# Kernel tuning notes

Measured on AMD Instinct MI355X. Metric: run time of the kernel, lower is better.

The kernel has to match this reference:

```python
import jax, jax.numpy as jnp
import numpy as np

NEG_SLOPE = 0.2


def _segment_softmax(scores, seg, num_segments):
    # scores: [nnz, H]; segment-wise (scatter) softmax, matching torch_geometric.utils.softmax
    m = jax.ops.segment_max(scores, seg, num_segments=num_segments)
    m = jnp.where(jnp.isfinite(m), m, 0.0)  # empty segments
    e = jnp.exp(scores - m[seg])
    s = jax.ops.segment_sum(e, seg, num_segments=num_segments)
    return e / (s[seg] + 1e-16)


def _class_partition(key, nnz, heads):
    # random permutation split into 4 class groups + inverse-permutation gather index
    perm = jax.random.permutation(key, nnz).astype(jnp.int32)
    q = nnz // 4
    parts = (perm[:q], perm[q:2 * q], perm[2 * q:3 * q], perm[3 * q:])
    inv = jnp.zeros((nnz,), jnp.int32).at[perm].set(jnp.arange(nnz, dtype=jnp.int32))
    gather_idx = jnp.broadcast_to(inv[:, None], (nnz, heads))
    return parts, gather_idx


def setup_inputs() -> dict:
    key = jax.random.key(0)
    N, M, NNZ = 100000, 50000, 800000
    IN_C, H, C = 128, 8, 16
    ks = jax.random.split(key, 9)
    X = jax.random.normal(ks[0], (N, IN_C), jnp.float32)
    vertex = jax.random.randint(ks[1], (NNZ,), 0, N, dtype=jnp.int32)
    edges = jax.random.randint(ks[2], (NNZ,), 0, M, dtype=jnp.int32)
    W_w = jax.random.normal(ks[3], (IN_C, H * C), jnp.float32) / np.float32(np.sqrt(IN_C))
    W_b = jnp.zeros((H * C,), jnp.float32)
    stdv = np.float32(np.sqrt(6.0 / (H + C)))
    att_e = jax.random.uniform(ks[4], (1, H, C), jnp.float32, -stdv, stdv)
    att_v = jax.random.uniform(ks[5], (1, H, C), jnp.float32, -stdv, stdv)
    (E0, E1, E2, E3), E_idx = _class_partition(ks[6], NNZ, H)
    (V0, V1, V2, V3), V_idx = _class_partition(ks[7], NNZ, H)
    return dict(X=X, vertex=vertex, edges=edges, W_w=W_w, W_b=W_b,
                att_e=att_e, att_v=att_v,
                E_class_index_0=E0, E_class_index_1=E1, E_class_index_2=E2, E_class_index_3=E3,
                E_class_index=E_idx,
                V_class_index_0=V0, V_class_index_1=V1, V_class_index_2=V2, V_class_index_3=V3,
                V_class_index=V_idx, edge_num=M)


def _class_scores(Xg, att, idx0, idx1, idx2, idx3):
    # (index_select by class, dot with att, sum over channel) then concat -> [nnz, H]
    parts = [jnp.sum(Xg[i] * att, axis=-1) for i in (idx0, idx1, idx2, idx3)]
    return jnp.concatenate(parts, axis=0)


def reference(X, vertex, edges, W_w, W_b, att_e, att_v,
              E_class_index_0, E_class_index_1, E_class_index_2, E_class_index_3, E_class_index,
              V_class_index_0, V_class_index_1, V_class_index_2, V_class_index_3, V_class_index,
              edge_num):
    N = X.shape[0]
    H, C = att_e.shape[1], att_e.shape[2]
    X0 = X @ W_w + W_b                       # [N, H*C]
    Xn = X0.reshape(N, H, C)
    Xve = Xn[vertex]                          # [nnz, H, C] gather node feats per incidence

    # vertex -> edge attention (edge-type-classed scores, segment softmax over hyperedges)
    Xe_cat = _class_scores(Xve, att_e, E_class_index_0, E_class_index_1, E_class_index_2, E_class_index_3)
    beta = jnp.take_along_axis(Xe_cat, E_class_index, axis=0)   # restore incidence order
    beta = jax.nn.leaky_relu(beta, NEG_SLOPE)
    beta = _segment_softmax(beta, edges, edge_num)              # [nnz, H]
    Xe = jax.ops.segment_sum(Xve * beta[..., None], edges, num_segments=edge_num)  # [M, H, C]
    Xe = jax.nn.relu(Xe)[edges]                                  # gather back: [nnz, H, C]

    # edge -> vertex attention (node-type-classed scores, segment softmax over vertices)
    Xa_cat = _class_scores(Xe, att_v, V_class_index_0, V_class_index_1, V_class_index_2, V_class_index_3)
    alpha = jnp.take_along_axis(Xa_cat, V_class_index, axis=0)
    alpha = jax.nn.leaky_relu(alpha, NEG_SLOPE)
    alpha = _segment_softmax(alpha, vertex, N)                   # [nnz, H]
    Xv = jax.ops.segment_sum(Xe * alpha[..., None], vertex, num_segments=N)  # [N, H, C]
    return Xv.reshape(N, H * C)
```

## Files before the change

### kernel.cpp

```cpp
#include <hip/hip_runtime.h>
#include <cstdint>
#include <cmath>

#define NEG_SLOPE 0.2f

static __device__ __forceinline__ float leaky(float x){ return x >= 0.f ? x : NEG_SLOPE*x; }

__global__ __launch_bounds__(256) void hist_rank_k(const int* __restrict__ edges, const int* __restrict__ vertex,
                                                   int* __restrict__ ce, int* __restrict__ cv,
                                                   int* __restrict__ re, int* __restrict__ rv, int nnz){
  int i = blockIdx.x*256 + threadIdx.x;
  if (i < nnz){
    re[i] = atomicAdd(&ce[edges[i]], 1);
    rv[i] = atomicAdd(&cv[vertex[i]], 1);
  }
}

__global__ __launch_bounds__(256) void scan_reduce_k(const int* __restrict__ ce, const int* __restrict__ cv,
                                                     int M, int N, int* __restrict__ partials){
  const int* src = blockIdx.y ? cv : ce;
  const int L = blockIdx.y ? N : M;
  const int base = blockIdx.x*2048;
  int s = 0;
  for (int j = threadIdx.x; j < 2048; j += 256){
    int idx = base + j;
    if (idx < L) s += src[idx];
  }
  for (int o = 32; o > 0; o >>= 1) s += __shfl_down(s, o);
  __shared__ int wsum[4];
  if ((threadIdx.x & 63) == 0) wsum[threadIdx.x >> 6] = s;
  __syncthreads();
  if (threadIdx.x == 0) partials[blockIdx.y*64 + blockIdx.x] = wsum[0]+wsum[1]+wsum[2]+wsum[3];
}

__global__ __launch_bounds__(128) void scan_partials_k(int* __restrict__ partials){
  const int w = threadIdx.x >> 6, l = threadIdx.x & 63;
  int v = partials[w*64 + l];
  int inc = v;
  for (int o = 1; o < 64; o <<= 1){ int u = __shfl_up(inc, o); if (l >= o) inc += u; }
  partials[w*64 + l] = inc - v;
}

__global__ __launch_bounds__(256) void scan_write_k(const int* __restrict__ ce, const int* __restrict__ cv,
                                                    int M, int N, const int* __restrict__ partials,
                                                    int* __restrict__ e_off, int* __restrict__ v_off){
  const int* src; int L; int* off;
  if (blockIdx.y == 0){ src = ce; L = M; off = e_off; }
  else                { src = cv; L = N; off = v_off; }
  const int base = blockIdx.x*2048 + threadIdx.x*8;
  int v[8];
  int tot = 0;
  #pragma unroll
  for (int j = 0; j < 8; ++j){ int idx = base+j; v[j] = (idx < L) ? src[idx] : 0; tot += v[j]; }
  const int lane = threadIdx.x & 63, wid = threadIdx.x >> 6;
  int inc = tot;
  for (int o = 1; o < 64; o <<= 1){ int u = __shfl_up(inc, o); if (lane >= o) inc += u; }
  __shared__ int wsum[4];
  if (lane == 63) wsum[wid] = inc;
  __syncthreads();
  int wbase = 0;
  for (int k = 0; k < wid; ++k) wbase += wsum[k];
  int run = partials[blockIdx.y*64 + blockIdx.x] + wbase + inc - tot;
  #pragma unroll
  for (int j = 0; j < 8; ++j){
    int idx = base + j;
    if (idx < L){
      off[idx] = run;
      run += v[j];
      if (idx == L-1) off[L] = run;
    }
  }
}

__global__ __launch_bounds__(256) void place_k(const int* __restrict__ edges, const int* __restrict__ vertex,
                                               const int* __restrict__ e_off, const int* __restrict__ v_off,
                                               const int* __restrict__ re, const int* __restrict__ rv,
                                               int* __restrict__ e_ent, int* __restrict__ v_ent, int nnz){
  int i = blockIdx.x*256 + threadIdx.x;
  if (i < nnz){
    atomicExch(&e_ent[e_off[edges[i]] + re[i]], i);
    atomicExch(&v_ent[v_off[vertex[i]] + rv[i]], i);
  }
}

__global__ __launch_bounds__(512) void gemm_k(const float* __restrict__ X, const float* __restrict__ W,
                                              const float* __restrict__ bias, const float* __restrict__ att_e,
                                              float* __restrict__ Y, float* __restrict__ sc_n, int N){
  __shared__ float Bs[64*128];
  __shared__ float As[64*65];
  __shared__ float att_s[128];
  const int t = threadIdx.x;
  if (t < 128) att_s[t] = att_e[t];
  const int row0 = blockIdx.x * 64;
  const int tr = t >> 4, tc = t & 15;
  const int r = tr*2, c = tc*8;
  float acc[2][8];
  {
    float4 b0 = ((const float4*)bias)[tc*2];
    float4 b1 = ((const float4*)bias)[tc*2+1];
    acc[0][0]=b0.x; acc[0][1]=b0.y; acc[0][2]=b0.z; acc[0][3]=b0.w;
    acc[0][4]=b1.x; acc[0][5]=b1.y; acc[0][6]=b1.z; acc[0][7]=b1.w;
    #pragma unroll
    for (int j = 0; j < 8; ++j) acc[1][j] = acc[0][j];
  }
  for (int kh = 0; kh < 2; ++kh){
    {
      const float4* W4 = (const float4*)(W + kh*64*128);
      float4* B4 = (float4*)Bs;
      #pragma unroll
      for (int j = 0; j < 4; ++j) B4[j*512 + t] = W4[j*512 + t];
      #pragma unroll
      for (int j = 0; j < 2; ++j){
        int idx = j*512 + t;
        int rr = idx >> 4, c4 = idx & 15;
        int gr = row0 + rr;
        float4 v = make_float4(0.f,0.f,0.f,0.f);
        if (gr < N) v = ((const float4*)X)[(size_t)gr*32 + kh*16 + c4];
        float* dst = &As[rr*65 + c4*4];
        dst[0]=v.x; dst[1]=v.y; dst[2]=v.z; dst[3]=v.w;
      }
    }
    __syncthreads();
    #pragma unroll 4
    for (int k = 0; k < 64; ++k){
      float a0 = As[r*65 + k], a1 = As[(r+1)*65 + k];
      const float4 w0 = *(const float4*)&Bs[k*128 + c];
      const float4 w1 = *(const float4*)&Bs[k*128 + c + 4];
      float wv[8] = {w0.x,w0.y,w0.z,w0.w,w1.x,w1.y,w1.z,w1.w};
      #pragma unroll
      for (int j = 0; j < 8; ++j){ acc[0][j] += a0*wv[j]; acc[1][j] += a1*wv[j]; }
    }
    __syncthreads();
  }
  float p0 = 0.f, p1 = 0.f;
  #pragma unroll
  for (int j = 0; j < 8; ++j){ p0 += acc[0][j]*att_s[c+j]; p1 += acc[1][j]*att_s[c+j]; }
  p0 += __shfl_xor(p0, 1);
  p1 += __shfl_xor(p1, 1);
  #pragma unroll
  for (int i = 0; i < 2; ++i){
    int gr = row0 + r + i;
    if (gr < N){
      float4 o0 = make_float4(acc[i][0],acc[i][1],acc[i][2],acc[i][3]);
      float4 o1 = make_float4(acc[i][4],acc[i][5],acc[i][6],acc[i][7]);
      float4* Y4 = (float4*)Y;
      Y4[(size_t)gr*32 + tc*2]     = o0;
      Y4[(size_t)gr*32 + tc*2 + 1] = o1;
    }
  }
  if ((tc & 1) == 0){
    int h = tc >> 1;
    int g0 = row0 + r, g1 = row0 + r + 1;
    if (g0 < N) sc_n[(size_t)g0*8 + h] = leaky(p0);
    if (g1 < N) sc_n[(size_t)g1*8 + h] = leaky(p1);
  }
}

template<bool RELU_SCORE>
__global__ __launch_bounds__(256) void agg_k(const float* __restrict__ src, const int* __restrict__ map,
                                             const float* __restrict__ sctab, const int* __restrict__ seg_off,
                                             const int* __restrict__ seg_ent, const float* __restrict__ att2,
                                             float* __restrict__ out, float* __restrict__ sc_out, int nseg){
  __shared__ float s_lds[4][128][8];
  __shared__ int   r_lds[4][128];
  __shared__ float m_lds[4][8];
  __shared__ float d_lds[4][8];
  __shared__ float att_s[128];
  const int wid = threadIdx.x >> 6, lane = threadIdx.x & 63;
  if (RELU_SCORE && threadIdx.x < 128) att_s[threadIdx.x] = att2[threadIdx.x];
  const int seg = blockIdx.x*4 + wid;
  const bool active = seg < nseg;
  int start = 0, cnt = 0;
  if (active){ start = seg_off[seg]; cnt = seg_off[seg+1] - start; }
  const bool fits = (cnt <= 128);

  if (active && fits){
    for (int j = lane; j < cnt; j += 64){
      int id = seg_ent[start + j];
      int row = map[id];
      r_lds[wid][j] = row;
      const float4* sp = (const float4*)(sctab + (size_t)row*8);
      float4 x0 = sp[0], x1 = sp[1];
      float* dst = &s_lds[wid][j][0];
      ((float4*)dst)[0] = x0;
      ((float4*)dst)[1] = x1;
    }
  }
  __syncthreads();
  if (active && fits){
    const int h = lane & 7, jj = lane >> 3;
    float m = -INFINITY;
    for (int j = jj; j < cnt; j += 8) m = fmaxf(m, s_lds[wid][j][h]);
    #pragma unroll
    for (int o = 8; o < 64; o <<= 1) m = fmaxf(m, __shfl_xor(m, o));
    float s = 0.f;
    for (int j = jj; j < cnt; j += 8) s += __expf(s_lds[wid][j][h] - m);
    #pragma unroll
    for (int o = 8; o < 64; o <<= 1) s += __shfl_xor(s, o);
    if (lane < 8){ m_lds[wid][lane] = m; d_lds[wid][lane] = 1.f / (s + 1e-16f); }
  }
  __syncthreads();
  if (active && fits){
    for (int idx = lane; idx < cnt*8; idx += 64){
      int j = idx >> 3, h = idx & 7;
      s_lds[wid][j][h] = __expf(s_lds[wid][j][h] - m_lds[wid][h]) * d_lds[wid][h];
    }
  }
  __syncthreads();
  if (active){
    float acc0 = 0.f, acc1 = 0.f;
    const int ha = lane >> 4, hb = ha + 4;
    if (fits){
      for (int j = 0; j < cnt; ++j){
        float wa = s_lds[wid][j][ha];
        float wb = s_lds[wid][j][hb];
        const float* xr = src + (size_t)r_lds[wid][j]*128;
        acc0 += wa * xr[lane];
        acc1 += wb * xr[lane + 64];
      }
    } else {
      float ma = -INFINITY, mb = -INFINITY;
      for (int j = 0; j < cnt; ++j){
        int id = seg_ent[start + j];
        int row = map[id];
        ma = fmaxf(ma, sctab[(size_t)row*8 + ha]);
        mb = fmaxf(mb, sctab[(size_t)row*8 + hb]);
      }
      float sa = 0.f, sb = 0.f;
      for (int j = 0; j < cnt; ++j){
        int id = seg_ent[start + j];
        int row = map[id];
        sa += __expf(sctab[(size_t)row*8 + ha] - ma);
        sb += __expf(sctab[(size_t)row*8 + hb] - mb);
      }
      float ra = 1.f/(sa + 1e-16f), rb = 1.f/(sb + 1e-16f);
      for (int j = 0; j < cnt; ++j){
        int id = seg_ent[start + j];
        int row = map[id];
        float wa = __expf(sctab[(size_t)row*8 + ha] - ma) * ra;
        float wb = __expf(sctab[(size_t)row*8 + hb] - mb) * rb;
        const float* xr = src + (size_t)row*128;
        acc0 += wa * xr[lane];
        acc1 += wb * xr[lane + 64];
      }
    }
    float o0 = RELU_SCORE ? fmaxf(acc0, 0.f) : acc0;
    float o1 = RELU_SCORE ? fmaxf(acc1, 0.f) : acc1;
    out[(size_t)seg*128 + lane]      = o0;
    out[(size_t)seg*128 + 64 + lane] = o1;
    if (RELU_SCORE){
      float p0 = o0 * att_s[lane];
      float p1 = o1 * att_s[lane + 64];
      #pragma unroll
      for (int o = 1; o < 16; o <<= 1){ p0 += __shfl_xor(p0, o); p1 += __shfl_xor(p1, o); }
      if ((lane & 15) == 0){
        sc_out[(size_t)seg*8 + (lane >> 4)]     = leaky(p0);
        sc_out[(size_t)seg*8 + 4 + (lane >> 4)] = leaky(p1);
      }
    }
  }
}

extern "C" void kernel_launch(void* const* d_in, const int* in_sizes, int n_in,
                              void* d_out, int out_size, void* d_ws, size_t ws_size,
                              hipStream_t stream){
  const float* X      = (const float*)d_in[0];
  const int*   vertex = (const int*)d_in[1];
  const int*   edges  = (const int*)d_in[2];
  const float* W_w    = (const float*)d_in[3];
  const float* W_b    = (const float*)d_in[4];
  const float* att_e  = (const float*)d_in[5];
  const float* att_v  = (const float*)d_in[6];
  const int N   = in_sizes[0] / 128;
  const int NNZ = in_sizes[1];
  const int M   = 50000;

  char* p = (char*)d_ws;
  auto take = [&](size_t bytes)->void*{
    void* q = (void*)p;
    p += (bytes + 255) & ~(size_t)255;
    return q;
  };
  float* X0       = (float*)take((size_t)N*128*sizeof(float));
  float* Xe       = (float*)take((size_t)M*128*sizeof(float));
  float* sc_n     = (float*)take((size_t)N*8*sizeof(float));
  float* sc_e     = (float*)take((size_t)M*8*sizeof(float));
  int*   e_off    = (int*)take((size_t)(M+1)*sizeof(int));
  int*   v_off    = (int*)take((size_t)(N+1)*sizeof(int));
  int*   e_cnt    = (int*)take((size_t)M*sizeof(int));
  int*   v_cnt    = (int*)take((size_t)N*sizeof(int));
  int*   re       = (int*)take((size_t)NNZ*sizeof(int));
  int*   rv       = (int*)take((size_t)NNZ*sizeof(int));
  int*   e_ent    = (int*)take((size_t)NNZ*sizeof(int));
  int*   v_ent    = (int*)take((size_t)NNZ*sizeof(int));
  int*   partials = (int*)take(128*sizeof(int));

  hipMemsetAsync(e_cnt, 0, (size_t)M*sizeof(int), stream);
  hipMemsetAsync(v_cnt, 0, (size_t)N*sizeof(int), stream);

  gemm_k<<<dim3((N+63)/64), 512, 0, stream>>>(X, W_w, W_b, att_e, X0, sc_n, N);

  hist_rank_k<<<dim3((NNZ+255)/256), 256, 0, stream>>>(edges, vertex, e_cnt, v_cnt, re, rv, NNZ);
  const int LMAX = (N > M) ? N : M;
  const int nb = (LMAX + 2047)/2048;
  scan_reduce_k<<<dim3(nb,2), 256, 0, stream>>>(e_cnt, v_cnt, M, N, partials);
  scan_partials_k<<<dim3(1), 128, 0, stream>>>(partials);
  scan_write_k<<<dim3(nb,2), 256, 0, stream>>>(e_cnt, v_cnt, M, N, partials, e_off, v_off);
  place_k<<<dim3((NNZ+255)/256), 256, 0, stream>>>(edges, vertex, e_off, v_off, re, rv, e_ent, v_ent, NNZ);

  agg_k<true><<<dim3((M+3)/4), 256, 0, stream>>>(X0, vertex, sc_n, e_off, e_ent, att_v, Xe, sc_e, M);

  agg_k<false><<<dim3((N+3)/4), 256, 0, stream>>>(Xe, edges, sc_e, v_off, v_ent, nullptr, (float*)d_out, nullptr, N);
}
```

Baseline: 524.1 us.

## Store intermediate Xe in bf16, use cursor atomics for CSR placement, remap GEMM columns

```diff
diff --git a/kernel.cpp b/kernel.cpp
--- a/kernel.cpp
+++ b/kernel.cpp
@@ -1,4 +1,5 @@
 #include <hip/hip_runtime.h>
+#include <hip/hip_bf16.h>
 #include <cstdint>
 #include <cmath>
 
@@ -6,14 +7,10 @@
 
 static __device__ __forceinline__ float leaky(float x){ return x >= 0.f ? x : NEG_SLOPE*x; }
 
-__global__ __launch_bounds__(256) void hist_rank_k(const int* __restrict__ edges, const int* __restrict__ vertex,
-                                                   int* __restrict__ ce, int* __restrict__ cv,
-                                                   int* __restrict__ re, int* __restrict__ rv, int nnz){
+__global__ __launch_bounds__(256) void hist_k(const int* __restrict__ edges, const int* __restrict__ vertex,
+                                              int* __restrict__ ce, int* __restrict__ cv, int nnz){
   int i = blockIdx.x*256 + threadIdx.x;
-  if (i < nnz){
-    re[i] = atomicAdd(&ce[edges[i]], 1);
-    rv[i] = atomicAdd(&cv[vertex[i]], 1);
-  }
+  if (i < nnz){ atomicAdd(&ce[edges[i]], 1); atomicAdd(&cv[vertex[i]], 1); }
 }
 
 __global__ __launch_bounds__(256) void scan_reduce_k(const int* __restrict__ ce, const int* __restrict__ cv,
@@ -41,10 +38,10 @@
   partials[w*64 + l] = inc - v;
 }
 
-__global__ __launch_bounds__(256) void scan_write_k(const int* __restrict__ ce, const int* __restrict__ cv,
+__global__ __launch_bounds__(256) void scan_write_k(int* __restrict__ ce, int* __restrict__ cv,
                                                     int M, int N, const int* __restrict__ partials,
                                                     int* __restrict__ e_off, int* __restrict__ v_off){
-  const int* src; int L; int* off;
+  int* src; int L; int* off;
   if (blockIdx.y == 0){ src = ce; L = M; off = e_off; }
   else                { src = cv; L = N; off = v_off; }
   const int base = blockIdx.x*2048 + threadIdx.x*8;
@@ -66,6 +63,7 @@
     int idx = base + j;
     if (idx < L){
       off[idx] = run;
+      src[idx] = run;
       run += v[j];
       if (idx == L-1) off[L] = run;
     }
@@ -73,13 +71,14 @@
 }
 
 __global__ __launch_bounds__(256) void place_k(const int* __restrict__ edges, const int* __restrict__ vertex,
-                                               const int* __restrict__ e_off, const int* __restrict__ v_off,
-                                               const int* __restrict__ re, const int* __restrict__ rv,
+                                               int* __restrict__ e_cur, int* __restrict__ v_cur,
                                                int* __restrict__ e_ent, int* __restrict__ v_ent, int nnz){
   int i = blockIdx.x*256 + threadIdx.x;
   if (i < nnz){
-    atomicExch(&e_ent[e_off[edges[i]] + re[i]], i);
-    atomicExch(&v_ent[v_off[vertex[i]] + rv[i]], i);
+    int p = atomicAdd(&e_cur[edges[i]], 1);
+    atomicExch(&e_ent[p], i);
+    int q = atomicAdd(&v_cur[vertex[i]], 1);
+    atomicExch(&v_ent[q], i);
   }
 }
 
@@ -93,11 +92,12 @@
   if (t < 128) att_s[t] = att_e[t];
   const int row0 = blockIdx.x * 64;
   const int tr = t >> 4, tc = t & 15;
-  const int r = tr*2, c = tc*8;
+  const int r = tr*2;
+  const int cA = tc*4, cB = 64 + tc*4;
   float acc[2][8];
   {
-    float4 b0 = ((const float4*)bias)[tc*2];
-    float4 b1 = ((const float4*)bias)[tc*2+1];
+    float4 b0 = ((const float4*)bias)[tc];
+    float4 b1 = ((const float4*)bias)[16 + tc];
     acc[0][0]=b0.x; acc[0][1]=b0.y; acc[0][2]=b0.z; acc[0][3]=b0.w;
     acc[0][4]=b1.x; acc[0][5]=b1.y; acc[0][6]=b1.z; acc[0][7]=b1.w;
     #pragma unroll
@@ -124,19 +124,26 @@
     #pragma unroll 4
     for (int k = 0; k < 64; ++k){
       float a0 = As[r*65 + k], a1 = As[(r+1)*65 + k];
-      const float4 w0 = *(const float4*)&Bs[k*128 + c];
-      const float4 w1 = *(const float4*)&Bs[k*128 + c + 4];
+      const float4 w0 = *(const float4*)&Bs[k*128 + cA];
+      const float4 w1 = *(const float4*)&Bs[k*128 + cB];
       float wv[8] = {w0.x,w0.y,w0.z,w0.w,w1.x,w1.y,w1.z,w1.w};
       #pragma unroll
       for (int j = 0; j < 8; ++j){ acc[0][j] += a0*wv[j]; acc[1][j] += a1*wv[j]; }
     }
     __syncthreads();
   }
-  float p0 = 0.f, p1 = 0.f;
-  #pragma unroll
-  for (int j = 0; j < 8; ++j){ p0 += acc[0][j]*att_s[c+j]; p1 += acc[1][j]*att_s[c+j]; }
-  p0 += __shfl_xor(p0, 1);
-  p1 += __shfl_xor(p1, 1);
+  float pA0=0.f, pA1=0.f, pB0=0.f, pB1=0.f;
+  #pragma unroll
+  for (int j = 0; j < 4; ++j){
+    float aa = att_s[cA + j], ab = att_s[cB + j];
+    pA0 += acc[0][j]*aa;   pA1 += acc[1][j]*aa;
+    pB0 += acc[0][4+j]*ab; pB1 += acc[1][4+j]*ab;
+  }
+  #pragma unroll
+  for (int o = 1; o < 4; o <<= 1){
+    pA0 += __shfl_xor(pA0, o); pA1 += __shfl_xor(pA1, o);
+    pB0 += __shfl_xor(pB0, o); pB1 += __shfl_xor(pB1, o);
+  }
   #pragma unroll
   for (int i = 0; i < 2; ++i){
     int gr = row0 + r + i;
@@ -144,30 +151,32 @@
       float4 o0 = make_float4(acc[i][0],acc[i][1],acc[i][2],acc[i][3]);
       float4 o1 = make_float4(acc[i][4],acc[i][5],acc[i][6],acc[i][7]);
       float4* Y4 = (float4*)Y;
-      Y4[(size_t)gr*32 + tc*2]     = o0;
-      Y4[(size_t)gr*32 + tc*2 + 1] = o1;
-    }
-  }
-  if ((tc & 1) == 0){
-    int h = tc >> 1;
+      Y4[(size_t)gr*32 + tc]      = o0;
+      Y4[(size_t)gr*32 + 16 + tc] = o1;
+    }
+  }
+  if ((tc & 3) == 0){
+    int h = tc >> 2;
     int g0 = row0 + r, g1 = row0 + r + 1;
-    if (g0 < N) sc_n[(size_t)g0*8 + h] = leaky(p0);
-    if (g1 < N) sc_n[(size_t)g1*8 + h] = leaky(p1);
-  }
-}
-
-template<bool RELU_SCORE>
-__global__ __launch_bounds__(256) void agg_k(const float* __restrict__ src, const int* __restrict__ map,
+    if (g0 < N){ sc_n[(size_t)g0*8 + h] = leaky(pA0); sc_n[(size_t)g0*8 + 4 + h] = leaky(pB0); }
+    if (g1 < N){ sc_n[(size_t)g1*8 + h] = leaky(pA1); sc_n[(size_t)g1*8 + 4 + h] = leaky(pB1); }
+  }
+}
+
+template<bool STAGE1>
+__global__ __launch_bounds__(256) void agg_k(const void* __restrict__ src_, const int* __restrict__ map,
                                              const float* __restrict__ sctab, const int* __restrict__ seg_off,
                                              const int* __restrict__ seg_ent, const float* __restrict__ att2,
-                                             float* __restrict__ out, float* __restrict__ sc_out, int nseg){
+                                             void* __restrict__ out_, float* __restrict__ sc_out, int nseg){
   __shared__ float s_lds[4][128][8];
   __shared__ int   r_lds[4][128];
   __shared__ float m_lds[4][8];
   __shared__ float d_lds[4][8];
   __shared__ float att_s[128];
+  const float* srcf = (const float*)src_;
+  const __hip_bfloat16* srcb = (const __hip_bfloat16*)src_;
   const int wid = threadIdx.x >> 6, lane = threadIdx.x & 63;
-  if (RELU_SCORE && threadIdx.x < 128) att_s[threadIdx.x] = att2[threadIdx.x];
+  if (STAGE1 && threadIdx.x < 128) att_s[threadIdx.x] = att2[threadIdx.x];
   const int seg = blockIdx.x*4 + wid;
   const bool active = seg < nseg;
   int start = 0, cnt = 0;
@@ -214,9 +223,16 @@
       for (int j = 0; j < cnt; ++j){
         float wa = s_lds[wid][j][ha];
         float wb = s_lds[wid][j][hb];
-        const float* xr = src + (size_t)r_lds[wid][j]*128;
-        acc0 += wa * xr[lane];
-        acc1 += wb * xr[lane + 64];
+        float x0, x1;
+        if (STAGE1){
+          const float* xr = srcf + (size_t)r_lds[wid][j]*128;
+          x0 = xr[lane]; x1 = xr[lane + 64];
+        } else {
+          const __hip_bfloat16* xr = srcb + (size_t)r_lds[wid][j]*128;
+          x0 = __bfloat162float(xr[lane]); x1 = __bfloat162float(xr[lane + 64]);
+        }
+        acc0 += wa * x0;
+        acc1 += wb * x1;
       }
     } else {
       float ma = -INFINITY, mb = -INFINITY;
@@ -239,16 +255,24 @@
         int row = map[id];
         float wa = __expf(sctab[(size_t)row*8 + ha] - ma) * ra;
         float wb = __expf(sctab[(size_t)row*8 + hb] - mb) * rb;
-        const float* xr = src + (size_t)row*128;
-        acc0 += wa * xr[lane];
-        acc1 += wb * xr[lane + 64];
-      }
-    }
-    float o0 = RELU_SCORE ? fmaxf(acc0, 0.f) : acc0;
-    float o1 = RELU_SCORE ? fmaxf(acc1, 0.f) : acc1;
-    out[(size_t)seg*128 + lane]      = o0;
-    out[(size_t)seg*128 + 64 + lane] = o1;
-    if (RELU_SCORE){
+        float x0, x1;
+        if (STAGE1){
+          const float* xr = srcf + (size_t)row*128;
+          x0 = xr[lane]; x1 = xr[lane + 64];
+        } else {
+          const __hip_bfloat16* xr = srcb + (size_t)row*128;
+          x0 = __bfloat162float(xr[lane]); x1 = __bfloat162float(xr[lane + 64]);
+        }
+        acc0 += wa * x0;
+        acc1 += wb * x1;
+      }
+    }
+    if (STAGE1){
+      float o0 = fmaxf(acc0, 0.f);
+      float o1 = fmaxf(acc1, 0.f);
+      __hip_bfloat16* outb = (__hip_bfloat16*)out_;
+      outb[(size_t)seg*128 + lane]      = __float2bfloat16(o0);
+      outb[(size_t)seg*128 + 64 + lane] = __float2bfloat16(o1);
       float p0 = o0 * att_s[lane];
       float p1 = o1 * att_s[lane + 64];
       #pragma unroll
@@ -257,6 +281,10 @@
         sc_out[(size_t)seg*8 + (lane >> 4)]     = leaky(p0);
         sc_out[(size_t)seg*8 + 4 + (lane >> 4)] = leaky(p1);
       }
+    } else {
+      float* outf = (float*)out_;
+      outf[(size_t)seg*128 + lane]      = acc0;
+      outf[(size_t)seg*128 + 64 + lane] = acc1;
     }
   }
 }
@@ -281,34 +309,32 @@
     p += (bytes + 255) & ~(size_t)255;
     return q;
   };
-  float* X0       = (float*)take((size_t)N*128*sizeof(float));
-  float* Xe       = (float*)take((size_t)M*128*sizeof(float));
-  float* sc_n     = (float*)take((size_t)N*8*sizeof(float));
-  float* sc_e     = (float*)take((size_t)M*8*sizeof(float));
-  int*   e_off    = (int*)take((size_t)(M+1)*sizeof(int));
-  int*   v_off    = (int*)take((size_t)(N+1)*sizeof(int));
-  int*   e_cnt    = (int*)take((size_t)M*sizeof(int));
-  int*   v_cnt    = (int*)take((size_t)N*sizeof(int));
-  int*   re       = (int*)take((size_t)NNZ*sizeof(int));
-  int*   rv       = (int*)take((size_t)NNZ*sizeof(int));
-  int*   e_ent    = (int*)take((size_t)NNZ*sizeof(int));
-  int*   v_ent    = (int*)take((size_t)NNZ*sizeof(int));
-  int*   partials = (int*)take(128*sizeof(int));
+  float* X0        = (float*)take((size_t)N*128*sizeof(float));
+  __hip_bfloat16* Xe = (__hip_bfloat16*)take((size_t)M*128*sizeof(__hip_bfloat16));
+  float* sc_n      = (float*)take((size_t)N*8*sizeof(float));
+  float* sc_e      = (float*)take((size_t)M*8*sizeof(float));
+  int*   e_off     = (int*)take((size_t)(M+1)*sizeof(int));
+  int*   v_off     = (int*)take((size_t)(N+1)*sizeof(int));
+  int*   e_cnt     = (int*)take((size_t)M*sizeof(int));
+  int*   v_cnt     = (int*)take((size_t)N*sizeof(int));
+  int*   e_ent     = (int*)take((size_t)NNZ*sizeof(int));
+  int*   v_ent     = (int*)take((size_t)NNZ*sizeof(int));
+  int*   partials  = (int*)take(128*sizeof(int));
 
   hipMemsetAsync(e_cnt, 0, (size_t)M*sizeof(int), stream);
   hipMemsetAsync(v_cnt, 0, (size_t)N*sizeof(int), stream);
 
   gemm_k<<<dim3((N+63)/64), 512, 0, stream>>>(X, W_w, W_b, att_e, X0, sc_n, N);
 
-  hist_rank_k<<<dim3((NNZ+255)/256), 256, 0, stream>>>(edges, vertex, e_cnt, v_cnt, re, rv, NNZ);
+  hist_k<<<dim3((NNZ+255)/256), 256, 0, stream>>>(edges, vertex, e_cnt, v_cnt, NNZ);
   const int LMAX = (N > M) ? N : M;
   const int nb = (LMAX + 2047)/2048;
   scan_reduce_k<<<dim3(nb,2), 256, 0, stream>>>(e_cnt, v_cnt, M, N, partials);
   scan_partials_k<<<dim3(1), 128, 0, stream>>>(partials);
   scan_write_k<<<dim3(nb,2), 256, 0, stream>>>(e_cnt, v_cnt, M, N, partials, e_off, v_off);
-  place_k<<<dim3((NNZ+255)/256), 256, 0, stream>>>(edges, vertex, e_off, v_off, re, rv, e_ent, v_ent, NNZ);
+  place_k<<<dim3((NNZ+255)/256), 256, 0, stream>>>(edges, vertex, e_cnt, v_cnt, e_ent, v_ent, NNZ);
 
   agg_k<true><<<dim3((M+3)/4), 256, 0, stream>>>(X0, vertex, sc_n, e_off, e_ent, att_v, Xe, sc_e, M);
 
-  agg_k<false><<<dim3((N+3)/4), 256, 0, stream>>>(Xe, edges, sc_e, v_off, v_ent, nullptr, (float*)d_out, nullptr, N);
-}
+  agg_k<false><<<dim3((N+3)/4), 256, 0, stream>>>(Xe, edges, sc_e, v_off, v_ent, nullptr, d_out, nullptr, N);
+}
```

Result: slower. 578.3 us (+10.3%).
